# Kernel optimization log

Measured on AMD Instinct MI355X. Metric: run time of the kernel, lower is better.

## Reference

```python
import jax, jax.numpy as jnp
import numpy as np

B, S, E, HD = 32, 1024, 768, 64
NUM_IMAGE_PATCHES = 49


def setup_inputs() -> dict:
    key = jax.random.key(0)
    ks = jax.random.split(key, 9)
    w = 0.02
    return {
        "decoder_sequence": jax.random.normal(ks[0], (B, S, E), dtype=jnp.float32),
        "Wq": jax.random.normal(ks[1], (E, HD), dtype=jnp.float32) * w,
        "bq": jnp.zeros((HD,), dtype=jnp.float32),
        "Wk": jax.random.normal(ks[2], (E, HD), dtype=jnp.float32) * w,
        "bk": jnp.zeros((HD,), dtype=jnp.float32),
        "Wv": jax.random.normal(ks[3], (E, HD), dtype=jnp.float32) * w,
        "bv": jnp.zeros((HD,), dtype=jnp.float32),
        "input_sequence_length": 975,
        "padding_mask": jax.random.randint(ks[4], (B, 1, S), 0, 2).astype(bool),
    }


def reference(decoder_sequence, Wq, bq, Wk, bk, Wv, bv, input_sequence_length, padding_mask):
    # single-head projections: [B,S,E] @ [E,HD] -> [B,S,HD]
    Q = decoder_sequence @ Wq + bq
    K = decoder_sequence @ Wk + bk
    V = decoder_sequence @ Wv + bv

    scores = jnp.einsum('bid,bjd->bij', Q, K) / jnp.sqrt(jnp.float32(HD))

    # mask: image-patch rows (i < 49) fully unmasked; text region is causal
    # (mask[49:,49:] = triu(-inf, diag=1)), i.e. -inf where i >= 49 and j > i.
    i = jnp.arange(S)[:, None]
    j = jnp.arange(S)[None, :]
    causal_bad = (i >= NUM_IMAGE_PATCHES) & (j > i)  # [S,S]
    scores = jnp.where(causal_bad[None, :, :], -jnp.inf, scores)

    # padding mask on keys, broadcast over queries: [B,1,S] -> [B,S,S]
    scores = jnp.where(padding_mask, -jnp.inf, scores)

    A = jax.nn.softmax(scores, axis=-1)
    H = jnp.einsum('bij,bjd->bid', A, V)
    return H
```

## Files before the change

### kernel.cpp

```cpp
#include <hip/hip_runtime.h>
#include <stdint.h>
#include <stddef.h>


typedef __attribute__((ext_vector_type(8))) short bf16x8;
typedef __attribute__((ext_vector_type(4))) float f32x4;

#define NIP 49
#define QSCALE 0.18033688011112042f

#define GLDS16(g, l)                                      \
  __builtin_amdgcn_global_load_lds(                       \
      (const __attribute__((address_space(1))) void*)(g), \
      (__attribute__((address_space(3))) void*)(l), 16, 0, 0)

__device__ __forceinline__ short f2b(float f) {
  union { float f; uint32_t u; } c; c.f = f;
  uint32_t u = c.u;
  uint32_t r = (u + 0x7fffu + ((u >> 16) & 1u)) >> 16;
  return (short)(uint16_t)r;
}

__device__ __forceinline__ uint32_t pk2(float lo, float hi) {
  uint32_t r;
  asm("v_cvt_pk_bf16_f32 %0, %1, %2" : "=v"(r) : "v"(lo), "v"(hi));
  return r;
}

__global__ __launch_bounds__(256) void wt_kernel(
    const float* __restrict__ Wq, const float* __restrict__ Wk,
    const float* __restrict__ Wv, const int* __restrict__ pad,
    short* __restrict__ Wt, float* __restrict__ padneg) {
  int e = blockIdx.x * 256 + threadIdx.x;
  int m = e / 49152;
  int r = e - m * 49152;
  int k = r >> 6, nl = r & 63;
  int n = m * 64 + nl;
  const float* W = (m == 0) ? Wq : (m == 1) ? Wk : Wv;
  const float v = W[r];
  int st = k >> 6, k64 = k & 63;
  int ks = k64 >> 5, k32 = k64 & 31;
  int t = (k32 >> 3) ^ ((n >> 1) & 3), b = k32 & 7;
  Wt[st * 12288 + ks * 6144 + n * 32 + t * 8 + b] = f2b(v);
  if (e < 32768) padneg[e] = pad[e] ? -16384.f : 0.f;
}

__global__ __launch_bounds__(256, 3) void proj_kernel(
    const float* __restrict__ X, const float* __restrict__ bq,
    const float* __restrict__ bk, const float* __restrict__ bv,
    const short* __restrict__ Wt, short* __restrict__ Qg,
    short* __restrict__ Kg, short* __restrict__ Vt) {
  __shared__ short lW[2][2][192][32];
  const int tid = threadIdx.x;
  const int wid = tid >> 6, lane = tid & 63;
  const int l15 = lane & 15, q4 = lane >> 4;
  const int r0 = blockIdx.x * 64;
  const int sig = (l15 >> 1) & 3;

  const float* xrow = X + (size_t)(r0 + wid * 16 + l15) * 768;
  float4 xa[2][4];
  auto xload = [&](int slot, int st) {
    const int kb = st * 64 + q4 * 8;
#pragma unroll
    for (int h = 0; h < 2; ++h) {
      xa[slot][h * 2 + 0] = *(const float4*)(xrow + kb + h * 32);
      xa[slot][h * 2 + 1] = *(const float4*)(xrow + kb + h * 32 + 4);
    }
  };
  auto mkfrag = [&](int slot, int h) {
    union { uint32_t u[4]; bf16x8 v; } r;
    const float4 a = xa[slot][h * 2], b = xa[slot][h * 2 + 1];
    r.u[0] = pk2(a.x, a.y); r.u[1] = pk2(a.z, a.w);
    r.u[2] = pk2(b.x, b.y); r.u[3] = pk2(b.z, b.w);
    return r.v;
  };

  auto wlds = [&](int buf, int st) {
    const short* src = Wt + (size_t)st * 12288 + lane * 8;
    short* dst = &lW[buf][0][0][0];
#pragma unroll
    for (int i = 0; i < 6; ++i) {
      const int g = wid * 6 + i;
      GLDS16(src + g * 512, dst + g * 512);
    }
  };

  f32x4 acc[12];
#pragma unroll
  for (int c = 0; c < 12; ++c) acc[c] = (f32x4){0.f, 0.f, 0.f, 0.f};

  wlds(0, 0);
  __builtin_amdgcn_sched_barrier(0);
  xload(0, 0);
  xload(1, 1);
  asm volatile("s_waitcnt vmcnt(8) lgkmcnt(0)" ::: "memory");
  __builtin_amdgcn_s_barrier();

#pragma unroll
  for (int st = 0; st < 12; ++st) {
    const int cur = st & 1;
    if (st + 1 < 12) {
      wlds(cur ^ 1, st + 1);
      __builtin_amdgcn_sched_barrier(0);
    }
    const bf16x8 a0 = mkfrag(cur, 0);
    const bf16x8 a1 = mkfrag(cur, 1);
    if (st + 2 < 12) xload(cur, st + 2);
#pragma unroll
    for (int ks = 0; ks < 2; ++ks) {
      const bf16x8 a = ks ? a1 : a0;
#pragma unroll
      for (int c = 0; c < 12; ++c) {
        const bf16x8 bw =
            *(const bf16x8*)&lW[cur][ks][c * 16 + l15][(q4 ^ sig) * 8];
        acc[c] = __builtin_amdgcn_mfma_f32_16x16x32_bf16(a, bw, acc[c], 0, 0, 0);
      }
    }
    if (st + 2 < 12)
      asm volatile("s_waitcnt vmcnt(4) lgkmcnt(0)" ::: "memory");
    else
      asm volatile("s_waitcnt vmcnt(0) lgkmcnt(0)" ::: "memory");
    __builtin_amdgcn_s_barrier();
  }

  const int b = r0 >> 10, s0 = r0 & 1023;
#pragma unroll
  for (int c = 0; c < 12; ++c) {
    const int mtx = c >> 2;
    const int h = (c & 3) * 16 + l15;
    if (mtx < 2) {
      const float bias = (mtx == 0 ? bq : bk)[h];
      short* op = (mtx == 0) ? Qg : Kg;
#pragma unroll
      for (int rr = 0; rr < 4; ++rr) {
        int row = r0 + wid * 16 + q4 * 4 + rr;
        float v = acc[c][rr] + bias;
        if (mtx == 0) v *= QSCALE;
        op[(size_t)row * 64 + h] = f2b(v);
      }
    } else {
      const float bias = bv[h];
      uint2 sv;
      sv.x = pk2(acc[c][0] + bias, acc[c][1] + bias);
      sv.y = pk2(acc[c][2] + bias, acc[c][3] + bias);
      *(uint2*)(Vt + ((size_t)(b * 64 + h) << 10) + s0 + wid * 16 + q4 * 4) = sv;
    }
  }
}

__global__ __launch_bounds__(256, 2) void attn_kernel(
    const short* __restrict__ Qg, const short* __restrict__ Kg,
    const short* __restrict__ Vt, const float* __restrict__ padneg,
    float* __restrict__ out) {
  __shared__ short lK[2][2][128][32];
  __shared__ short lV[2][4][64][32];
  __shared__ short lOnes[16][32];

  const int b = blockIdx.x;
  const int level = blockIdx.y;
  const int t = (level == 0) ? 0 : 16 - level;
  const int tid = threadIdx.x;
  const int wid = tid >> 6, lane = tid & 63;
  const int l15 = lane & 15, q4 = lane >> 4;
  const int qs = t * 64;
  const size_t base = (size_t)b * 1024;
  const int nkt = (t == 0) ? 8 : (t / 2 + 1);

  {
    int i0 = tid, i1 = tid + 256;
    ((short*)lOnes)[i0] = ((i0 >> 5) == 0) ? (short)0x3F80 : (short)0;
    if (i1 < 512) ((short*)lOnes)[i1] = ((i1 >> 5) == 0) ? (short)0x3F80 : (short)0;
  }

  const short* qrow = Qg + (base + qs + wid * 16 + l15) * 64;
  bf16x8 bq0 = *(const bf16x8*)(qrow + q4 * 8);
  bf16x8 bq1 = *(const bf16x8*)(qrow + 32 + q4 * 8);
  const int qi = qs + wid * 16 + l15;

  const int sr = lane >> 2, sc = (lane & 3) * 8;
  auto wlds_tile = [&](int buf, int kt) {
    const int kb = kt * 128;
#pragma unroll
    for (int i = 0; i < 4; ++i) {
      const int dh = i & 1, krow = wid * 32 + (i >> 1) * 16;
      GLDS16(Kg + (base + kb + krow + sr) * 64 + dh * 32 + sc,
             &lK[buf][dh][krow][0]);
    }
#pragma unroll
    for (int kq = 0; kq < 4; ++kq) {
      GLDS16(Vt + ((size_t)(b * 64 + wid * 16 + sr) << 10) + kb + kq * 32 + sc,
             &lV[buf][kq][wid * 16][0]);
    }
  };

  float4 pnv[8];
  auto pnload = [&](int kt) {
#pragma unroll
    for (int c = 0; c < 8; ++c)
      pnv[c] = *(const float4*)(padneg + base + kt * 128 + c * 16 + q4 * 4);
  };

  pnload(0);
  wlds_tile(0, 0);
  __syncthreads();

  f32x4 o[5];
#pragma unroll
  for (int c = 0; c < 5; ++c) o[c] = (f32x4){0.f, 0.f, 0.f, 0.f};

  for (int kt = 0; kt < nkt; ++kt) {
    const int cur = kt & 1;
    const int kb = kt * 128;

    f32x4 s4[8];
#pragma unroll
    for (int c = 0; c < 8; ++c)
      s4[c] = (f32x4){pnv[c].x, pnv[c].y, pnv[c].z, pnv[c].w};

    if (kt + 1 < nkt) {
      wlds_tile(cur ^ 1, kt + 1);
      pnload(kt + 1);
    }

#pragma unroll
    for (int c = 0; c < 8; ++c) {
      bf16x8 a0 = *(const bf16x8*)&lK[cur][0][c * 16 + l15][q4 * 8];
      s4[c] = __builtin_amdgcn_mfma_f32_16x16x32_bf16(a0, bq0, s4[c], 0, 0, 0);
      bf16x8 a1 = *(const bf16x8*)&lK[cur][1][c * 16 + l15][q4 * 8];
      s4[c] = __builtin_amdgcn_mfma_f32_16x16x32_bf16(a1, bq1, s4[c], 0, 0, 0);
    }

    const bool diag = (t == 0) ? (kt == 0) : (kt == nkt - 1);
    const bool img = (t == 0 && kt > 0);
#pragma unroll
    for (int c = 0; c < 8; ++c) {
#pragma unroll
      for (int rr = 0; rr < 4; ++rr) {
        float pv = exp2f(fminf(s4[c][rr], 80.f));
        if (diag) {
          int j = kb + c * 16 + q4 * 4 + rr;
          if (qi >= NIP && j > qi) pv = 0.f;
        }
        if (img) {
          if (qi >= NIP) pv = 0.f;
        }
        s4[c][rr] = pv;
      }
    }

#pragma unroll
    for (int m = 0; m < 4; ++m) {
      uint32_t w0 = pk2(s4[2 * m][0], s4[2 * m][1]);
      uint32_t w1 = pk2(s4[2 * m][2], s4[2 * m][3]);
      uint32_t w2 = pk2(s4[2 * m + 1][0], s4[2 * m + 1][1]);
      uint32_t w3 = pk2(s4[2 * m + 1][2], s4[2 * m + 1][3]);
      asm("v_permlane32_swap_b32 %0, %1" : "+v"(w0), "+v"(w2));
      asm("v_permlane32_swap_b32 %0, %1" : "+v"(w1), "+v"(w3));
      asm("v_permlane16_swap_b32 %0, %1" : "+v"(w0), "+v"(w2));
      asm("v_permlane16_swap_b32 %0, %1" : "+v"(w1), "+v"(w3));
      union { uint32_t u[4]; bf16x8 v; } af;
      af.u[0] = w0; af.u[1] = w1; af.u[2] = w2; af.u[3] = w3;
#pragma unroll
      for (int c = 0; c < 5; ++c) {
        bf16x8 bv = (c < 4) ? *(const bf16x8*)&lV[cur][m][c * 16 + l15][q4 * 8]
                            : *(const bf16x8*)&lOnes[l15][q4 * 8];
        o[c] = __builtin_amdgcn_mfma_f32_16x16x32_bf16(af.v, bv, o[c], 0, 0, 0);
      }
    }
    __syncthreads();
  }

#pragma unroll
  for (int rr = 0; rr < 4; ++rr) {
    float l = __shfl(o[4][rr], lane & 48, 64);
    const float inv = (l > 0.f) ? 1.0f / l : 0.f;
    const size_t row = base + qs + wid * 16 + q4 * 4 + rr;
#pragma unroll
    for (int c = 0; c < 4; ++c)
      out[row * 64 + c * 16 + l15] = o[c][rr] * inv;
  }
}

extern "C" void kernel_launch(void* const* d_in, const int* in_sizes, int n_in,
                              void* d_out, int out_size, void* d_ws, size_t ws_size,
                              hipStream_t stream) {
  const float* X  = (const float*)d_in[0];
  const float* Wq = (const float*)d_in[1];
  const float* bq = (const float*)d_in[2];
  const float* Wk = (const float*)d_in[3];
  const float* bk = (const float*)d_in[4];
  const float* Wv = (const float*)d_in[5];
  const float* bv = (const float*)d_in[6];
  const int* pad  = (const int*)d_in[8];
  float* out = (float*)d_out;

  short* Qg = (short*)d_ws;
  short* Kg = Qg + 32768 * 64;
  short* Vt = Kg + 32768 * 64;
  short* Wt = Vt + 32768 * 64;
  float* padneg = (float*)(Wt + 147456);

  wt_kernel<<<576, 256, 0, stream>>>(Wq, Wk, Wv, pad, Wt, padneg);
  proj_kernel<<<512, 256, 0, stream>>>(X, bq, bk, bv, Wt, Qg, Kg, Vt);
  attn_kernel<<<dim3(32, 16), 256, 0, stream>>>(Qg, Kg, Vt, padneg, out);
}
```

Measured before the change: 198.0 us.

## Stream K/V chunks straight into registers and drop LDS staging in attention

The attention kernel no longer stages K and V tiles through double-buffered shared memory with block-wide barriers. Each wave now loads 32-key chunks of K, V and the padding bias straight from global memory into two register buffers that alternate. The causal loop bound moves from 128-key tiles to 32-key chunks, which trims wasted work on the diagonal. The softmax denominator is summed in fp32 on the vector units with lane shuffles, replacing the extra ones-vector MFMA. The cost is that each wave re-reads the same K/V data from cache instead of sharing it through LDS, and the occupancy hint in the launch bounds is removed.

Result: slower. 224.6 us (+13.4%).

```diff
diff --git a/kernel.cpp b/kernel.cpp
--- a/kernel.cpp
+++ b/kernel.cpp
@@ -25,6 +25,12 @@
   uint32_t r;
   asm("v_cvt_pk_bf16_f32 %0, %1, %2" : "=v"(r) : "v"(lo), "v"(hi));
   return r;
+}
+
+__device__ __forceinline__ float pexp(float s, bool mf, int qi, int j) {
+  float pv = exp2f(fminf(s, 80.f));
+  if (mf && qi >= NIP && j > qi) pv = 0.f;
+  return pv;
 }
 
 __global__ __launch_bounds__(256) void wt_kernel(
@@ -148,14 +154,64 @@
   }
 }
 
-__global__ __launch_bounds__(256, 2) void attn_kernel(
+
+#define CHLOAD(S, KC)                                                          \
+  do {                                                                         \
+    const int kb_ = (KC) * 32;                                                 \
+    ka##S[0] = *(const bf16x8*)(kbase + (size_t)(kb_ + 0) * 64 + 0);           \
+    ka##S[1] = *(const bf16x8*)(kbase + (size_t)(kb_ + 0) * 64 + 32);          \
+    ka##S[2] = *(const bf16x8*)(kbase + (size_t)(kb_ + 16) * 64 + 0);          \
+    ka##S[3] = *(const bf16x8*)(kbase + (size_t)(kb_ + 16) * 64 + 32);         \
+    pn##S[0] = *(const float4*)(pnbase + kb_);                                 \
+    pn##S[1] = *(const float4*)(pnbase + kb_ + 16);                            \
+    va##S[0] = *(const bf16x8*)(vbase + kb_);                                  \
+    va##S[1] = *(const bf16x8*)(vbase + 16384 + kb_);                          \
+    va##S[2] = *(const bf16x8*)(vbase + 32768 + kb_);                          \
+    va##S[3] = *(const bf16x8*)(vbase + 49152 + kb_);                          \
+    __builtin_amdgcn_sched_barrier(0);                                         \
+  } while (0)
+
+#define COMPUTE(S, KC)                                                         \
+  do {                                                                         \
+    const int kb_ = (KC) * 32;                                                 \
+    f32x4 s0_ = (f32x4){pn##S[0].x, pn##S[0].y, pn##S[0].z, pn##S[0].w};       \
+    f32x4 s1_ = (f32x4){pn##S[1].x, pn##S[1].y, pn##S[1].z, pn##S[1].w};       \
+    s0_ = __builtin_amdgcn_mfma_f32_16x16x32_bf16(ka##S[0], bq0, s0_, 0, 0, 0);\
+    s0_ = __builtin_amdgcn_mfma_f32_16x16x32_bf16(ka##S[1], bq1, s0_, 0, 0, 0);\
+    s1_ = __builtin_amdgcn_mfma_f32_16x16x32_bf16(ka##S[2], bq0, s1_, 0, 0, 0);\
+    s1_ = __builtin_amdgcn_mfma_f32_16x16x32_bf16(ka##S[3], bq1, s1_, 0, 0, 0);\
+    const bool mf_ = (kb_ + 31 > thr);                                         \
+    float p0_[4], p1_[4];                                                      \
+    p0_[0] = pexp(s0_[0], mf_, qi, kb_ + q4 * 4 + 0);                          \
+    p0_[1] = pexp(s0_[1], mf_, qi, kb_ + q4 * 4 + 1);                          \
+    p0_[2] = pexp(s0_[2], mf_, qi, kb_ + q4 * 4 + 2);                          \
+    p0_[3] = pexp(s0_[3], mf_, qi, kb_ + q4 * 4 + 3);                          \
+    p1_[0] = pexp(s1_[0], mf_, qi, kb_ + 16 + q4 * 4 + 0);                     \
+    p1_[1] = pexp(s1_[1], mf_, qi, kb_ + 16 + q4 * 4 + 1);                     \
+    p1_[2] = pexp(s1_[2], mf_, qi, kb_ + 16 + q4 * 4 + 2);                     \
+    p1_[3] = pexp(s1_[3], mf_, qi, kb_ + 16 + q4 * 4 + 3);                     \
+    lsum += ((p0_[0] + p0_[1]) + (p0_[2] + p0_[3])) +                          \
+            ((p1_[0] + p1_[1]) + (p1_[2] + p1_[3]));                           \
+    uint32_t w0_ = pk2(p0_[0], p0_[1]);                                        \
+    uint32_t w1_ = pk2(p0_[2], p0_[3]);                                        \
+    uint32_t w2_ = pk2(p1_[0], p1_[1]);                                        \
+    uint32_t w3_ = pk2(p1_[2], p1_[3]);                                        \
+    asm("v_permlane32_swap_b32 %0, %1" : "+v"(w0_), "+v"(w2_));                \
+    asm("v_permlane32_swap_b32 %0, %1" : "+v"(w1_), "+v"(w3_));                \
+    asm("v_permlane16_swap_b32 %0, %1" : "+v"(w0_), "+v"(w2_));                \
+    asm("v_permlane16_swap_b32 %0, %1" : "+v"(w1_), "+v"(w3_));                \
+    union { uint32_t u[4]; bf16x8 v; } af_;                                    \
+    af_.u[0] = w0_; af_.u[1] = w1_; af_.u[2] = w2_; af_.u[3] = w3_;            \
+    o[0] = __builtin_amdgcn_mfma_f32_16x16x32_bf16(af_.v, va##S[0], o[0], 0, 0, 0); \
+    o[1] = __builtin_amdgcn_mfma_f32_16x16x32_bf16(af_.v, va##S[1], o[1], 0, 0, 0); \
+    o[2] = __builtin_amdgcn_mfma_f32_16x16x32_bf16(af_.v, va##S[2], o[2], 0, 0, 0); \
+    o[3] = __builtin_amdgcn_mfma_f32_16x16x32_bf16(af_.v, va##S[3], o[3], 0, 0, 0); \
+  } while (0)
+
+__global__ __launch_bounds__(256) void attn_kernel(
     const short* __restrict__ Qg, const short* __restrict__ Kg,
     const short* __restrict__ Vt, const float* __restrict__ padneg,
     float* __restrict__ out) {
-  __shared__ short lK[2][2][128][32];
-  __shared__ short lV[2][4][64][32];
-  __shared__ short lOnes[16][32];
-
   const int b = blockIdx.x;
   const int level = blockIdx.y;
   const int t = (level == 0) ? 0 : 16 - level;
@@ -164,115 +220,43 @@
   const int l15 = lane & 15, q4 = lane >> 4;
   const int qs = t * 64;
   const size_t base = (size_t)b * 1024;
-  const int nkt = (t == 0) ? 8 : (t / 2 + 1);
-
-  {
-    int i0 = tid, i1 = tid + 256;
-    ((short*)lOnes)[i0] = ((i0 >> 5) == 0) ? (short)0x3F80 : (short)0;
-    if (i1 < 512) ((short*)lOnes)[i1] = ((i1 >> 5) == 0) ? (short)0x3F80 : (short)0;
-  }
+  const int nkc = (t == 0) ? 32 : 2 * (t + 1);
 
   const short* qrow = Qg + (base + qs + wid * 16 + l15) * 64;
-  bf16x8 bq0 = *(const bf16x8*)(qrow + q4 * 8);
-  bf16x8 bq1 = *(const bf16x8*)(qrow + 32 + q4 * 8);
+  const bf16x8 bq0 = *(const bf16x8*)(qrow + q4 * 8);
+  const bf16x8 bq1 = *(const bf16x8*)(qrow + 32 + q4 * 8);
   const int qi = qs + wid * 16 + l15;
-
-  const int sr = lane >> 2, sc = (lane & 3) * 8;
-  auto wlds_tile = [&](int buf, int kt) {
-    const int kb = kt * 128;
-#pragma unroll
-    for (int i = 0; i < 4; ++i) {
-      const int dh = i & 1, krow = wid * 32 + (i >> 1) * 16;
-      GLDS16(Kg + (base + kb + krow + sr) * 64 + dh * 32 + sc,
-             &lK[buf][dh][krow][0]);
-    }
-#pragma unroll
-    for (int kq = 0; kq < 4; ++kq) {
-      GLDS16(Vt + ((size_t)(b * 64 + wid * 16 + sr) << 10) + kb + kq * 32 + sc,
-             &lV[buf][kq][wid * 16][0]);
-    }
-  };
-
-  float4 pnv[8];
-  auto pnload = [&](int kt) {
-#pragma unroll
-    for (int c = 0; c < 8; ++c)
-      pnv[c] = *(const float4*)(padneg + base + kt * 128 + c * 16 + q4 * 4);
-  };
-
-  pnload(0);
-  wlds_tile(0, 0);
-  __syncthreads();
-
-  f32x4 o[5];
-#pragma unroll
-  for (int c = 0; c < 5; ++c) o[c] = (f32x4){0.f, 0.f, 0.f, 0.f};
-
-  for (int kt = 0; kt < nkt; ++kt) {
-    const int cur = kt & 1;
-    const int kb = kt * 128;
-
-    f32x4 s4[8];
-#pragma unroll
-    for (int c = 0; c < 8; ++c)
-      s4[c] = (f32x4){pnv[c].x, pnv[c].y, pnv[c].z, pnv[c].w};
-
-    if (kt + 1 < nkt) {
-      wlds_tile(cur ^ 1, kt + 1);
-      pnload(kt + 1);
-    }
-
-#pragma unroll
-    for (int c = 0; c < 8; ++c) {
-      bf16x8 a0 = *(const bf16x8*)&lK[cur][0][c * 16 + l15][q4 * 8];
-      s4[c] = __builtin_amdgcn_mfma_f32_16x16x32_bf16(a0, bq0, s4[c], 0, 0, 0);
-      bf16x8 a1 = *(const bf16x8*)&lK[cur][1][c * 16 + l15][q4 * 8];
-      s4[c] = __builtin_amdgcn_mfma_f32_16x16x32_bf16(a1, bq1, s4[c], 0, 0, 0);
-    }
-
-    const bool diag = (t == 0) ? (kt == 0) : (kt == nkt - 1);
-    const bool img = (t == 0 && kt > 0);
-#pragma unroll
-    for (int c = 0; c < 8; ++c) {
-#pragma unroll
-      for (int rr = 0; rr < 4; ++rr) {
-        float pv = exp2f(fminf(s4[c][rr], 80.f));
-        if (diag) {
-          int j = kb + c * 16 + q4 * 4 + rr;
-          if (qi >= NIP && j > qi) pv = 0.f;
-        }
-        if (img) {
-          if (qi >= NIP) pv = 0.f;
-        }
-        s4[c][rr] = pv;
-      }
-    }
-
-#pragma unroll
-    for (int m = 0; m < 4; ++m) {
-      uint32_t w0 = pk2(s4[2 * m][0], s4[2 * m][1]);
-      uint32_t w1 = pk2(s4[2 * m][2], s4[2 * m][3]);
-      uint32_t w2 = pk2(s4[2 * m + 1][0], s4[2 * m + 1][1]);
-      uint32_t w3 = pk2(s4[2 * m + 1][2], s4[2 * m + 1][3]);
-      asm("v_permlane32_swap_b32 %0, %1" : "+v"(w0), "+v"(w2));
-      asm("v_permlane32_swap_b32 %0, %1" : "+v"(w1), "+v"(w3));
-      asm("v_permlane16_swap_b32 %0, %1" : "+v"(w0), "+v"(w2));
-      asm("v_permlane16_swap_b32 %0, %1" : "+v"(w1), "+v"(w3));
-      union { uint32_t u[4]; bf16x8 v; } af;
-      af.u[0] = w0; af.u[1] = w1; af.u[2] = w2; af.u[3] = w3;
-#pragma unroll
-      for (int c = 0; c < 5; ++c) {
-        bf16x8 bv = (c < 4) ? *(const bf16x8*)&lV[cur][m][c * 16 + l15][q4 * 8]
-                            : *(const bf16x8*)&lOnes[l15][q4 * 8];
-        o[c] = __builtin_amdgcn_mfma_f32_16x16x32_bf16(af.v, bv, o[c], 0, 0, 0);
-      }
-    }
-    __syncthreads();
-  }
-
+  const int thr = (t == 0) ? ((wid == 3) ? NIP : 0x7fffffff) : (qs + wid * 16);
+
+  const short* kbase = Kg + (base + l15) * 64 + q4 * 8;
+  const short* vbase = Vt + ((size_t)(b * 64 + l15) << 10) + q4 * 8;
+  const float* pnbase = padneg + base + q4 * 4;
+
+  bf16x8 ka0[4], ka1[4], va0[4], va1[4];
+  float4 pn0[2], pn1[2];
+  f32x4 o[4];
+#pragma unroll
+  for (int c = 0; c < 4; ++c) o[c] = (f32x4){0.f, 0.f, 0.f, 0.f};
+  float lsum = 0.f;
+
+  CHLOAD(0, 0);
+  int kc = 0;
+  while (true) {
+    if (kc + 1 < nkc) CHLOAD(1, kc + 1);
+    COMPUTE(0, kc);
+    ++kc;
+    if (kc >= nkc) break;
+    if (kc + 1 < nkc) CHLOAD(0, kc + 1);
+    COMPUTE(1, kc);
+    ++kc;
+    if (kc >= nkc) break;
+  }
+
+  lsum += __shfl_xor(lsum, 16);
+  lsum += __shfl_xor(lsum, 32);
 #pragma unroll
   for (int rr = 0; rr < 4; ++rr) {
-    float l = __shfl(o[4][rr], lane & 48, 64);
+    const float l = __shfl(lsum, q4 * 4 + rr);
     const float inv = (l > 0.f) ? 1.0f / l : 0.f;
     const size_t row = base + qs + wid * 16 + q4 * 4 + rr;
 #pragma unroll
```
